# Optimization experiments

Hardware: AMD Instinct MI355X
Metric: run time of the kernel (lower is better)

## Reference

```python
import jax, jax.numpy as jnp
import numpy as np

B, N, TOPK = 64, 1024, 32
C1, DQ, DH, DO, DMLP = 92, 256, 512, 256, 1024
BN_EPS = 1e-5


def setup_inputs() -> dict:
    key = jax.random.key(0)
    ks = jax.random.split(key, 12)
    d_in = DQ + C1 + 4  # 352: query_embed + probs + bbox
    return {
        "probs": jax.random.normal(ks[0], (B, N, C1), jnp.float32),
        "bbox_coords": jax.random.uniform(ks[1], (B, N, 4), jnp.float32),
        "query_emb": jax.random.normal(ks[2], (N, DQ), jnp.float32),
        "node_emb": jax.random.normal(ks[3], (N, DQ), jnp.float32),
        "mlp_w1": jax.random.normal(ks[4], (d_in, DMLP), jnp.float32) * 0.02,
        "mlp_b1": jnp.zeros((DMLP,), jnp.float32),
        "mlp_w2": jax.random.normal(ks[5], (DMLP, N), jnp.float32) * 0.02,
        "mlp_b2": jnp.zeros((N,), jnp.float32),
        "conv1_w": jax.random.normal(ks[6], (DQ, DH), jnp.float32) * (DQ ** -0.5),
        "conv1_b": jnp.zeros((DH,), jnp.float32),
        "conv2_w": jax.random.normal(ks[7], (DH, DO), jnp.float32) * (DH ** -0.5),
        "conv2_b": jnp.zeros((DO,), jnp.float32),
        "bn_gamma": jnp.ones((DH,), jnp.float32),
        "bn_beta": jnp.zeros((DH,), jnp.float32),
    }


def reference(probs, bbox_coords, query_emb, node_emb, mlp_w1, mlp_b1,
              mlp_w2, mlp_b2, conv1_w, conv1_b, conv2_w, conv2_b,
              bn_gamma, bn_beta):
    b = probs.shape[0]
    # edge-weight MLP (2 layers, relu after first) -> dense adjacency (B,N,N)
    x = jnp.concatenate([jnp.broadcast_to(query_emb[None], (b, N, DQ)), probs, bbox_coords], axis=-1)
    adj = jax.nn.relu(x @ mlp_w1 + mlp_b1) @ mlp_w2 + mlp_b2
    vals, idx = jax.lax.top_k(adj, TOPK)          # (B,N,K) values sorted desc
    cols = idx.reshape(b, -1)                      # (B, N*K) targets
    w = vals.reshape(b, -1)                        # (B, N*K) edge weights
    loop = jnp.arange(N)
    row = jnp.repeat(loop, TOPK)                   # (N*K,) sources, shared
    rows_all = jnp.concatenate([row, loop])        # self-loops appended (fill=1)

    def gcn(xw, bias, c, ww):
        # GCNConv: sym-normalized gather-scale-scatter over edges + self loops
        cols2 = jnp.concatenate([c, loop])
        w2 = jnp.concatenate([ww, jnp.ones((N,), xw.dtype)])
        deg = jax.ops.segment_sum(w2, cols2, num_segments=N)
        dinv = deg ** -0.5
        dinv = jnp.where(jnp.isinf(dinv), 0.0, dinv)
        norm = dinv[rows_all] * w2 * dinv[cols2]
        return jax.ops.segment_sum(norm[:, None] * xw[rows_all], cols2, num_segments=N) + bias

    xw1 = node_emb @ conv1_w                       # shared across batch

    def per_batch(c, ww):
        h = gcn(xw1, conv1_b, c, ww)               # (N, DH)
        mu = h.mean(0)
        var = h.var(0)                             # biased var, as torch BN
        h = (h - mu) / jnp.sqrt(var + BN_EPS) * bn_gamma + bn_beta
        h = jax.nn.relu(h)
        return gcn(h @ conv2_w, conv2_b, c, ww)    # (N, DO)

    out = jax.vmap(per_batch)(cols, w)             # (B, N, DO)
    return out[:, None]                            # (B, 1, N, DO) matches torch stack of unsqueezed outs
```

## Files before the change

kernel.cpp:

```cpp
#include <hip/hip_runtime.h>
#include <stdint.h>

typedef float f32x4 __attribute__((ext_vector_type(4)));
typedef _Float16 h16x8 __attribute__((ext_vector_type(8)));
typedef _Float16 h16;
typedef unsigned short u16;

#define WSYNC() do { asm volatile("s_waitcnt lgkmcnt(0)" ::: "memory"); \
  __builtin_amdgcn_sched_barrier(0); } while (0)


__global__ void k_split_t(const float* __restrict__ in, h16* __restrict__ out,
                          int Cn, int Ck, int ostride, int doSplit) {
  __shared__ float t[32][33];
  int n0 = blockIdx.x * 32, k0 = blockIdx.y * 32;
  int tx = threadIdx.x, ty = threadIdx.y;
#pragma unroll
  for (int i = 0; i < 4; ++i)
    t[ty + i * 8][tx] = in[(size_t)(k0 + ty + i * 8) * Cn + n0 + tx];
  __syncthreads();
#pragma unroll
  for (int i = 0; i < 4; ++i) {
    int n = n0 + ty + i * 8, k = k0 + tx;
    float v = t[tx][ty + i * 8];
    h16 h = (h16)v;
    size_t base = (size_t)n * ostride + k;
    out[base] = h;
    if (doSplit) {
      out[base + Ck] = h;
      out[base + 2 * Ck] = (h16)(v - (float)h);
    }
  }
}

__global__ void k_xcat(const float* __restrict__ qe, const float* __restrict__ probs,
                       const float* __restrict__ bbox, h16* __restrict__ x, int r0, int n) {
  int i = blockIdx.x * 256 + threadIdx.x;
  if (i >= n) return;
  int rl = i / 352, k = i - rl * 352;
  int R = r0 + rl;
  int nn = R & 1023;
  float v;
  if (k < 256)      v = qe[nn * 256 + k];
  else if (k < 348) v = probs[(size_t)R * 92 + (k - 256)];
  else              v = bbox[(size_t)R * 4 + (k - 348)];
  h16 h = (h16)v;
  h16 l = (h16)(v - (float)h);
  size_t base = (size_t)rl * 704;
  x[base + k] = h; x[base + 352 + k] = l;
}

__global__ void k_xw1(const float* __restrict__ ne, const float* __restrict__ c1w,
                      float* __restrict__ xw1f) {
  int r = blockIdx.x >> 1;
  int d = (blockIdx.x & 1) * 256 + threadIdx.x;
  float s = 0.0f;
  for (int k = 0; k < 256; ++k) s += ne[r * 256 + k] * c1w[k * 512 + d];
  xw1f[r * 512 + d] = s;
}


template<int MODE>
__global__ __launch_bounds__(512, 2)
void k_gemm8(const h16* __restrict__ A, const h16* __restrict__ B, void* __restrict__ Cptr,
             const float* __restrict__ bias, const float* __restrict__ rscale,
             float2* __restrict__ bnp, int M, int N, int K, int AK) {
  __shared__ __align__(16) char lds[131072];
  const int tid = threadIdx.x;
  const int lane = tid & 63, wid = tid >> 6;
  const int wr = wid >> 2, wc = wid & 3;

  const int gx = N >> 8;
  const int nwg = gridDim.x, wg = blockIdx.x;
  const int q8 = nwg >> 3, r8 = nwg & 7, xcd = wg & 7, lo = wg >> 3;
  const int swz = (xcd < r8 ? xcd * (q8 + 1) : r8 * (q8 + 1) + (xcd - r8) * q8) + lo;
  const int bx = swz % gx, by = swz / gx;

  const int nt = K >> 6;
  const int srow = tid >> 3, s8 = tid & 7;

  char* ldsA = (char*)lds;
  char* ldsB = (char*)lds + 65536;

  auto stage = [&](const h16* __restrict__ Mat, int rowStride, int tileRowBase,
                   char* ldsBase, int buf, int half, int kbase) {
#pragma unroll
    for (int j = 0; j < 2; ++j) {
      int rl = half * 128 + srow + j * 64;
      int gcol = kbase + ((s8 ^ (rl & 7)) << 3);
      const char* src = (const char*)(Mat + (size_t)(tileRowBase + rl) * rowStride + gcol);
      char* dst = ldsBase + buf * 32768 + half * 16384 + j * 8192 + tid * 16;
      __builtin_amdgcn_global_load_lds((const __attribute__((address_space(1))) void*)src,
                                       (__attribute__((address_space(3))) void*)dst, 16, 0, 0);
    }
  };

  f32x4 acc[8][4] = {};
  h16x8 bfr[4][2];

  auto rdA = [&](int buf, int mf, int ks) -> h16x8 {
    int row = wr * 128 + mf * 16 + (lane & 15);
    int cb = ((ks << 6) + ((lane >> 4) << 4)) ^ ((row & 7) << 4);
    return *(const h16x8*)(ldsA + buf * 32768 + row * 128 + cb);
  };
  auto rdB = [&](int buf, int nf, int ks) -> h16x8 {
    int row = wc * 64 + nf * 16 + (lane & 15);
    int cb = ((ks << 6) + ((lane >> 4) << 4)) ^ ((row & 7) << 4);
    return *(const h16x8*)(ldsB + buf * 32768 + row * 128 + cb);
  };

#define BARRIER() do { asm volatile("" ::: "memory"); \
  __builtin_amdgcn_s_barrier(); asm volatile("" ::: "memory"); } while (0)

#define MFMA16(q, af)                                                          \
  __builtin_amdgcn_s_setprio(1);                                               \
  _Pragma("unroll") for (int m2 = 0; m2 < 2; ++m2)                             \
  _Pragma("unroll") for (int nf = 0; nf < 4; ++nf)                             \
  _Pragma("unroll") for (int ks = 0; ks < 2; ++ks)                             \
    acc[(q) * 2 + m2][nf] = __builtin_amdgcn_mfma_f32_16x16x32_f16(            \
        af[m2][ks], bfr[nf][ks], acc[(q) * 2 + m2][nf], 0, 0, 0);              \
  __builtin_amdgcn_s_setprio(0);

  const int aRow = by * 256, bRow = bx * 256;

  stage(A, AK, aRow, ldsA, 0, 0, 0);
  stage(A, AK, aRow, ldsA, 0, 1, 0);
  stage(B, K, bRow, ldsB, 0, 0, 0);
  stage(B, K, bRow, ldsB, 0, 1, 0);
  stage(B, K, bRow, ldsB, 1, 0, 64);
  stage(B, K, bRow, ldsB, 1, 1, 64);
  asm volatile("s_waitcnt vmcnt(4)" ::: "memory");
  BARRIER();

  for (int T = 0; T < nt; ++T) {
    const int p = T & 1;
    const int tkA = (T + 1) << 6;
    const int aA = (tkA < AK) ? tkA : tkA - AK;
    const int tkB = (T + 2) << 6;
    const bool sA = (T + 1) < nt, sB = (T + 2) < nt;

    {
#pragma unroll
      for (int nf = 0; nf < 4; ++nf)
#pragma unroll
        for (int ks = 0; ks < 2; ++ks) bfr[nf][ks] = rdB(p, nf, ks);
      h16x8 af[2][2];
#pragma unroll
      for (int m2 = 0; m2 < 2; ++m2)
#pragma unroll
        for (int ks = 0; ks < 2; ++ks) af[m2][ks] = rdA(p, m2, ks);
      if (sA) stage(A, AK, aRow, ldsA, p ^ 1, 0, aA);
      BARRIER();
      MFMA16(0, af)
      BARRIER();
    }
    {
      h16x8 af[2][2];
#pragma unroll
      for (int m2 = 0; m2 < 2; ++m2)
#pragma unroll
        for (int ks = 0; ks < 2; ++ks) af[m2][ks] = rdA(p, 2 + m2, ks);
      if (sA) stage(A, AK, aRow, ldsA, p ^ 1, 1, aA);
      BARRIER();
      MFMA16(1, af)
      BARRIER();
    }
    {
      h16x8 af[2][2];
#pragma unroll
      for (int m2 = 0; m2 < 2; ++m2)
#pragma unroll
        for (int ks = 0; ks < 2; ++ks) af[m2][ks] = rdA(p, 4 + m2, ks);
      if (sB) stage(B, K, bRow, ldsB, p, 0, tkB);
      BARRIER();
      MFMA16(2, af)
      BARRIER();
    }
    {
      h16x8 af[2][2];
#pragma unroll
      for (int m2 = 0; m2 < 2; ++m2)
#pragma unroll
        for (int ks = 0; ks < 2; ++ks) af[m2][ks] = rdA(p, 6 + m2, ks);
      if (sB) stage(B, K, bRow, ldsB, p, 1, tkB);
      BARRIER();
      MFMA16(3, af)
      if (sB) { asm volatile("s_waitcnt vmcnt(4)" ::: "memory"); }
      else    { asm volatile("s_waitcnt vmcnt(0)" ::: "memory"); }
      BARRIER();
    }
  }

  const int tM = by * 256 + wr * 128, tN = bx * 256 + wc * 64;
  float sl[4] = {0.f, 0.f, 0.f, 0.f}, ssl[4] = {0.f, 0.f, 0.f, 0.f};
#pragma unroll
  for (int mf = 0; mf < 8; ++mf) {
#pragma unroll
    for (int nf = 0; nf < 4; ++nf) {
      int c = tN + nf * 16 + (lane & 15);
      float bvl = bias[c];
#pragma unroll
      for (int i = 0; i < 4; ++i) {
        int r = tM + mf * 16 + (lane >> 4) * 4 + i;
        float v = acc[mf][nf][i];
        if (MODE == 5) v = v * rscale[r] + bvl;
        else v += bvl;
        if (MODE == 2) {
          ((float*)Cptr)[(size_t)r * N + c] = v;
        } else if (MODE == 5) {
          ((h16*)Cptr)[(size_t)r * N + c] = (h16)v;
          sl[nf] += v; ssl[nf] += v * v;
        } else {
          v = fmaxf(v, 0.0f);
          h16 h = (h16)v;
          h16 l = (h16)(v - (float)h);
          size_t o = (size_t)r * (2 * N) + c;
          ((h16*)Cptr)[o] = h;
          ((h16*)Cptr)[o + N] = l;
        }
      }
    }
  }
  if (MODE == 5) {
    int b = by >> 2;
#pragma unroll
    for (int nf = 0; nf < 4; ++nf) {
      float s = sl[nf], ss = ssl[nf];
      s += __shfl_xor(s, 16); ss += __shfl_xor(ss, 16);
      s += __shfl_xor(s, 32); ss += __shfl_xor(ss, 32);
      if (lane < 16) {
        int c = tN + nf * 16 + lane;
        atomicAdd(&bnp[b * 512 + c].x, s);
        atomicAdd(&bnp[b * 512 + c].y, ss);
      }
    }
  }
#undef BARRIER
#undef MFMA16
}


template<int MODE, int RELU>
__global__ __launch_bounds__(256)
void k_gemm(const h16* __restrict__ A, const h16* __restrict__ B, void* __restrict__ Cptr,
            const float* __restrict__ bias, const float* __restrict__ rscale,
            int M, int N, int K, int AK, int gx,
            long long sA, long long sB, long long sC) {
  __shared__ __align__(16) h16 As[128 * 32];
  __shared__ __align__(16) h16 Bs[128 * 32];
  const int tid = threadIdx.x;
  const int wid = tid >> 6, lane = tid & 63;
  const int wr = wid >> 1, wc = wid & 1;
  const int bz = blockIdx.y;

  const int nwg = gridDim.x, wg = blockIdx.x;
  const int q = nwg >> 3, r8 = nwg & 7, xcd = wg & 7, lo = wg >> 3;
  const int swz = (xcd < r8 ? xcd * (q + 1) : r8 * (q + 1) + (xcd - r8) * q) + lo;
  const int bx = swz % gx, by = swz / gx;

  const char* gA = (const char*)(A + (size_t)bz * sA + (size_t)by * 128 * AK +
                                 (size_t)(tid >> 2) * AK) + (tid & 3) * 16;
  const char* gB = (const char*)(B + (size_t)bz * sB + (size_t)bx * 128 * K +
                                 (size_t)(tid >> 2) * K) + (tid & 3) * 16;
  char* lAs = (char*)As + wid * 1024;
  char* lBs = (char*)Bs + wid * 1024;
  const long long rowStepA = (long long)64 * AK * 2;
  const long long rowStepB = (long long)64 * K * 2;

  f32x4 acc[4][4] = {};
  const int aoff = (wr * 64 + (lane & 15)) * 32 + (lane >> 4) * 8;
  const int boff = (wc * 64 + (lane & 15)) * 32 + (lane >> 4) * 8;

  for (int kt = 0; kt < K; kt += 32) {
    const int akt = (kt < AK) ? kt : kt - AK;
    __syncthreads();
#pragma unroll
    for (int j = 0; j < 2; ++j) {
      __builtin_amdgcn_global_load_lds(
          (const __attribute__((address_space(1))) void*)(gA + j * rowStepA + (size_t)akt * 2),
          (__attribute__((address_space(3))) void*)(lAs + j * 4096), 16, 0, 0);
      __builtin_amdgcn_global_load_lds(
          (const __attribute__((address_space(1))) void*)(gB + j * rowStepB + (size_t)kt * 2),
          (__attribute__((address_space(3))) void*)(lBs + j * 4096), 16, 0, 0);
    }
    asm volatile("s_waitcnt vmcnt(0)" ::: "memory");
    __syncthreads();

    h16x8 af[4], bv[4];
#pragma unroll
    for (int m = 0; m < 4; ++m) af[m] = *(const h16x8*)(As + aoff + m * 512);
#pragma unroll
    for (int n = 0; n < 4; ++n) bv[n] = *(const h16x8*)(Bs + boff + n * 512);
#pragma unroll
    for (int m = 0; m < 4; ++m)
#pragma unroll
      for (int n = 0; n < 4; ++n)
        acc[m][n] = __builtin_amdgcn_mfma_f32_16x16x32_f16(af[m], bv[n], acc[m][n], 0, 0, 0);
  }

  const int tM = by * 128 + wr * 64, tN = bx * 128 + wc * 64;
#pragma unroll
  for (int m = 0; m < 4; ++m) {
#pragma unroll
    for (int n = 0; n < 4; ++n) {
      int c = tN + n * 16 + (lane & 15);
      float bvl = bias ? bias[c] : 0.0f;
#pragma unroll
      for (int i = 0; i < 4; ++i) {
        int r = tM + m * 16 + (lane >> 4) * 4 + i;
        float v = acc[m][n][i];
        if (rscale) v *= rscale[bz * 1024 + r];
        v += bvl;
        if (RELU) v = fmaxf(v, 0.0f);
        if (MODE == 1) {
          size_t o = ((size_t)(r >> 10) * N + c) * 1024 + (r & 1023);
          ((h16*)Cptr)[o] = (h16)v;
        } else if (MODE == 2) {
          size_t o = (size_t)bz * sC + (size_t)r * N + c;
          ((float*)Cptr)[o] = v;
        }
      }
    }
  }
}


__global__ void k_topk(const float* __restrict__ adj, float* __restrict__ vals,
                       u16* __restrict__ idxo, float* __restrict__ deg, int r0) {
  __shared__ unsigned binsAll[4][256];
  const int wv = threadIdx.x >> 6, lane = threadIdx.x & 63;
  unsigned* bins = binsAll[wv];
  const int rl = blockIdx.x * 4 + wv;

  float v[16]; unsigned key[16];
  const float4* rp = (const float4*)(adj + (size_t)rl * 1024 + lane * 16);
#pragma unroll
  for (int q = 0; q < 4; ++q) {
    float4 t = rp[q];
    v[4 * q] = t.x; v[4 * q + 1] = t.y; v[4 * q + 2] = t.z; v[4 * q + 3] = t.w;
  }
#pragma unroll
  for (int j = 0; j < 16; ++j) {
    unsigned b = __float_as_uint(v[j]);
    key[j] = b ^ (unsigned)(((int)b >> 31) | (int)0x80000000);
  }

  unsigned pfx = 0; int need = 32;
#pragma unroll
  for (int lvl = 0; lvl < 4; ++lvl) {
    const int shift = 24 - lvl * 8;
    bins[lane] = 0; bins[lane + 64] = 0; bins[lane + 128] = 0; bins[lane + 192] = 0;
    WSYNC();
#pragma unroll
    for (int j = 0; j < 16; ++j) {
      bool cand = (lvl == 0) || ((key[j] >> (shift + 8)) == pfx);
      if (cand) atomicAdd(&bins[(key[j] >> shift) & 255u], 1u);
    }
    WSYNC();
    int c0 = (int)bins[lane * 4 + 0], c1 = (int)bins[lane * 4 + 1],
        c2 = (int)bins[lane * 4 + 2], c3 = (int)bins[lane * 4 + 3];
    WSYNC();
    int s = c0 + c1 + c2 + c3;
    int inc = s;
#pragma unroll
    for (int off = 1; off < 64; off <<= 1) {
      int t = __shfl_down(inc, off);
      if (lane + off < 64) inc += t;
    }
    int gt3 = inc - s;
    int gt2 = gt3 + c3, gt1 = gt2 + c2, gt0 = gt1 + c1;
    int tloc = -1, gtsel = 0;
    if (gt3 < need && gt3 + c3 >= need) { tloc = lane * 4 + 3; gtsel = gt3; }
    if (gt2 < need && gt2 + c2 >= need) { tloc = lane * 4 + 2; gtsel = gt2; }
    if (gt1 < need && gt1 + c1 >= need) { tloc = lane * 4 + 1; gtsel = gt1; }
    if (gt0 < need && gt0 + c0 >= need) { tloc = lane * 4 + 0; gtsel = gt0; }
    unsigned long long bal = __ballot(tloc >= 0);
    int src = __ffsll(bal) - 1;
    int t   = __shfl(tloc, src);
    int gtv = __shfl(gtsel, src);
    pfx = (pfx << 8) | (unsigned)t;
    need -= gtv;
  }

  unsigned sureMask = 0, tieMask = 0;
#pragma unroll
  for (int j = 0; j < 16; ++j) {
    if (key[j] > pfx) sureMask |= (1u << j);
    else if (key[j] == pfx) tieMask |= (1u << j);
  }
  int cs = __popc(sureMask), ct = __popc(tieMask);
  int incS = cs, incT = ct;
#pragma unroll
  for (int off = 1; off < 64; off <<= 1) {
    int a = __shfl_up(incS, off);
    int b2 = __shfl_up(incT, off);
    if (lane >= off) { incS += a; incT += b2; }
  }
  int baseS = incS - cs, baseT = incT - ct;
  int totalS = __shfl(incS, 63);
  size_t obase = ((size_t)(r0 + rl)) * 32;
  int degb = ((r0 + rl) >> 10) << 10;
  int o = baseS;
#pragma unroll
  for (int j = 0; j < 16; ++j)
    if (sureMask & (1u << j)) {
      vals[obase + o] = v[j];
      idxo[obase + o] = (u16)(lane * 16 + j);
      atomicAdd(&deg[degb + lane * 16 + j], v[j]);
      ++o;
    }
  int o2 = totalS + baseT;
#pragma unroll
  for (int j = 0; j < 16; ++j)
    if (tieMask & (1u << j)) {
      if (o2 < 32) {
        vals[obase + o2] = v[j];
        idxo[obase + o2] = (u16)(lane * 16 + j);
        atomicAdd(&deg[degb + lane * 16 + j], v[j]);
      }
      ++o2;
    }
}


__global__ void k_deg_init(float* deg) {
  int i = blockIdx.x * 256 + threadIdx.x;
  if (i < 65536) deg[i] = 1.0f;
}

__global__ void k_dinv(const float* __restrict__ deg, float* __restrict__ dinv) {
  int i = blockIdx.x * 256 + threadIdx.x;
  if (i >= 65536) return;
  float d = deg[i];
  float r = 1.0f / sqrtf(d);
  if (isinf(r)) r = 0.0f;
  dinv[i] = r;
}

__global__ void k_self(const float* __restrict__ dinv, h16* __restrict__ Wd, int g) {
  int i = blockIdx.x * 256 + threadIdx.x;
  if (i >= 16384) return;
  int bl = i >> 10, c = i & 1023;
  Wd[((size_t)bl << 20) + (size_t)c * 1024 + c] = (h16)dinv[g * 16384 + i];
}

__global__ void k_edge(const float* __restrict__ vals, const u16* __restrict__ idxo,
                       const float* __restrict__ dinv, h16* __restrict__ Wd, int g) {
  int e = blockIdx.x * 256 + threadIdx.x;
  if (e >= 524288) return;
  int bl = e >> 15;
  int r = (e >> 5) & 1023;
  size_t E = (size_t)g * 524288 + e;
  int c = (int)idxo[E];
  float w = vals[E] * dinv[g * 16384 + (bl << 10) + r];
  size_t o = ((size_t)bl << 20) + (size_t)c * 1024 + r;
  Wd[o] = (h16)((float)Wd[o] + w);
}

__global__ void k_wipe(const u16* __restrict__ idxo, h16* __restrict__ Wd, int g) {
  int t = blockIdx.x * 256 + threadIdx.x;
  if (t < 524288) {
    int bl = t >> 15, r = (t >> 5) & 1023;
    int c = (int)idxo[(size_t)g * 524288 + t];
    Wd[((size_t)bl << 20) + (size_t)c * 1024 + r] = (h16)0.0f;
  } else {
    int i = t - 524288;
    if (i < 16384) {
      int bl = i >> 10, c = i & 1023;
      Wd[((size_t)bl << 20) + (size_t)c * 1024 + c] = (h16)0.0f;
    }
  }
}


__global__ void k_bnfin(const float2* __restrict__ part, float* __restrict__ mu,
                        float* __restrict__ rstd) {
  int i = blockIdx.x * 256 + threadIdx.x;
  if (i >= 8192) return;
  float2 t = part[i];
  float m = t.x * (1.0f / 1024.0f);
  float var = t.y * (1.0f / 1024.0f) - m * m;
  mu[i] = m;
  rstd[i] = 1.0f / sqrtf(var + 1e-5f);
}

__global__ void k_bnapply(h16* __restrict__ h1, const float* __restrict__ mu,
                          const float* __restrict__ rstd, const float* __restrict__ gamma,
                          const float* __restrict__ beta) {
  int i = blockIdx.x * 256 + threadIdx.x;
  if (i >= 16 * 1024 * 512) return;
  int d = i & 511;
  int b = i >> 19;
  float y = ((float)h1[i] - mu[b * 512 + d]) * rstd[b * 512 + d] * gamma[d] + beta[d];
  h1[i] = (h16)fmaxf(y, 0.0f);
}


extern "C" void kernel_launch(void* const* d_in, const int* in_sizes, int n_in,
                              void* d_out, int out_size, void* d_ws, size_t ws_size,
                              hipStream_t stream) {
  const float* probs = (const float*)d_in[0];
  const float* bbox  = (const float*)d_in[1];
  const float* qe    = (const float*)d_in[2];
  const float* ne    = (const float*)d_in[3];
  const float* w1    = (const float*)d_in[4];
  const float* b1    = (const float*)d_in[5];
  const float* w2    = (const float*)d_in[6];
  const float* b2    = (const float*)d_in[7];
  const float* c1w   = (const float*)d_in[8];
  const float* c1b   = (const float*)d_in[9];
  const float* c2w   = (const float*)d_in[10];
  const float* c2b   = (const float*)d_in[11];
  const float* gamma = (const float*)d_in[12];
  const float* beta  = (const float*)d_in[13];

  if (ws_size < 82444288ULL) return;
  const bool big = ws_size >= 115998720ULL;
  const int CH = big ? 16384 : 8192;
  const int NCH = 65536 / CH;

  char* p = (char*)d_ws;
  h16* W1cat = (h16*)p; p += (size_t)1024 * 1088 * 2;
  h16* W2cat = (h16*)p; p += (size_t)1024 * 3072 * 2;
  h16* c2wt  = (h16*)p; p += (size_t)256 * 512 * 2;
  float* xw1f = (float*)p; p += (size_t)1024 * 512 * 4;
  h16*  xw1t = (h16*)p;  p += (size_t)512 * 1024 * 2;
  float* vals = (float*)p; p += (size_t)2097152 * 4;
  u16*   idxo = (u16*)p;   p += (size_t)2097152 * 2;
  float* deg  = (float*)p; p += (size_t)65536 * 4;
  float* dinv = (float*)p; p += (size_t)65536 * 4;
  float* mu   = (float*)p; p += (size_t)64 * 512 * 4;
  float* rstd = (float*)p; p += (size_t)64 * 512 * 4;
  float2* bnp = (float2*)p; p += (size_t)16 * 8 * 512 * 8;
  char* R1 = p;
  h16* Xcat  = (h16*)R1;
  h16* Hcat2 = (h16*)(R1 + (size_t)CH * 704 * 2);
  h16* Wd   = (h16*)R1;
  h16* h1   = (h16*)(R1 + 33554432);
  h16* xw2t = (h16*)(R1 + 50331648);
  float* adjf = (float*)d_out;

  hipMemsetAsync(W1cat, 0, (size_t)1024 * 1088 * 2, stream);
  k_split_t<<<dim3(32, 11), dim3(32, 8), 0, stream>>>(w1, W1cat, 1024, 352, 1088, 1);
  k_split_t<<<dim3(32, 32), dim3(32, 8), 0, stream>>>(w2, W2cat, 1024, 1024, 3072, 1);
  k_split_t<<<dim3(8, 16), dim3(32, 8), 0, stream>>>(c2w, c2wt, 256, 512, 512, 0);
  k_xw1<<<2048, 256, 0, stream>>>(ne, c1w, xw1f);
  k_split_t<<<dim3(16, 32), dim3(32, 8), 0, stream>>>(xw1f, xw1t, 512, 1024, 1024, 0);
  k_deg_init<<<256, 256, 0, stream>>>(deg);

  for (int c = 0; c < NCH; ++c) {
    int r0 = c * CH;
    k_xcat<<<(CH * 352) / 256, 256, 0, stream>>>(qe, probs, bbox, Xcat, r0, CH * 352);
    k_gemm8<3><<<(CH / 256) * 4, 512, 0, stream>>>(Xcat, W1cat, Hcat2, b1, nullptr,
                                                   nullptr, CH, 1024, 1088, 704);
    k_gemm8<2><<<(CH / 256) * 4, 512, 0, stream>>>(Hcat2, W2cat, adjf, b2, nullptr,
                                                   nullptr, CH, 1024, 3072, 2048);
    k_topk<<<CH / 4, 256, 0, stream>>>(adjf, vals, idxo, deg, r0);
  }

  k_dinv<<<256, 256, 0, stream>>>(deg, dinv);

  for (int g = 0; g < 4; ++g) {
    const float* dg = dinv + g * 16384;
    if (g == 0) hipMemsetAsync(Wd, 0, (size_t)33554432, stream);
    k_self<<<64, 256, 0, stream>>>(dinv, Wd, g);
    k_edge<<<2048, 256, 0, stream>>>(vals, idxo, dinv, Wd, g);
    hipMemsetAsync(bnp, 0, (size_t)16 * 512 * 8, stream);
    k_gemm8<5><<<128, 512, 0, stream>>>(Wd, xw1t, h1, c1b, dg, bnp,
                                        16384, 512, 1024, 1024);
    k_bnfin<<<32, 256, 0, stream>>>(bnp, mu, rstd);
    k_bnapply<<<32768, 256, 0, stream>>>(h1, mu, rstd, gamma, beta);
    k_gemm<1, 0><<<dim3(256, 1), 256, 0, stream>>>(h1, c2wt, xw2t, nullptr, nullptr,
                                                   16384, 256, 512, 512, 2, 0, 0, 0);
    k_gemm<2, 0><<<dim3(16, 16), 256, 0, stream>>>(Wd, xw2t,
                                                   (float*)d_out + (size_t)g * 16 * 262144,
                                                   c2b, dg, 1024, 256, 1024, 1024, 2,
                                                   1048576LL, 262144LL, 262144LL);
    if (g < 3) k_wipe<<<2112, 256, 0, stream>>>(idxo, Wd, g);
  }
}
```

Baseline: 1.454 ms.

## Route GCN second-layer GEMMs through the pipelined 256x256 kernel with batch strides

Adds batch strides and an optional row scale/bias to the large double-buffered 256x256 MFMA GEMM, plus a transposed-output mode. The two small 128x128 GEMMs in the second GCN layer now use it instead of the simpler kernel, which is removed. BN apply is vectorised to 8 halves per thread. The sparse wipe kernel is replaced by a full 32MB memset every group, which adds memory traffic. The second-layer GEMMs also launch far fewer workgroups (64 blocks for the xw2 GEMM), which may underfill the GPU.

```diff
diff --git a/kernel.cpp b/kernel.cpp
--- a/kernel.cpp
+++ b/kernel.cpp
@@ -64,11 +64,13 @@
 __global__ __launch_bounds__(512, 2)
 void k_gemm8(const h16* __restrict__ A, const h16* __restrict__ B, void* __restrict__ Cptr,
              const float* __restrict__ bias, const float* __restrict__ rscale,
-             float2* __restrict__ bnp, int M, int N, int K, int AK) {
+             float2* __restrict__ bnp, int M, int N, int K, int AK,
+             long long sA, long long sB, long long sC) {
   __shared__ __align__(16) char lds[131072];
   const int tid = threadIdx.x;
   const int lane = tid & 63, wid = tid >> 6;
   const int wr = wid >> 2, wc = wid & 3;
+  const int bz = blockIdx.y;
 
   const int gx = N >> 8;
   const int nwg = gridDim.x, wg = blockIdx.x;
@@ -78,6 +80,9 @@
 
   const int nt = K >> 6;
   const int srow = tid >> 3, s8 = tid & 7;
+
+  const h16* Ab = A + (size_t)bz * sA;
+  const h16* Bb = B + (size_t)bz * sB;
 
   char* ldsA = (char*)lds;
   char* ldsB = (char*)lds + 65536;
@@ -123,12 +128,12 @@
 
   const int aRow = by * 256, bRow = bx * 256;
 
-  stage(A, AK, aRow, ldsA, 0, 0, 0);
-  stage(A, AK, aRow, ldsA, 0, 1, 0);
-  stage(B, K, bRow, ldsB, 0, 0, 0);
-  stage(B, K, bRow, ldsB, 0, 1, 0);
-  stage(B, K, bRow, ldsB, 1, 0, 64);
-  stage(B, K, bRow, ldsB, 1, 1, 64);
+  stage(Ab, AK, aRow, ldsA, 0, 0, 0);
+  stage(Ab, AK, aRow, ldsA, 0, 1, 0);
+  stage(Bb, K, bRow, ldsB, 0, 0, 0);
+  stage(Bb, K, bRow, ldsB, 0, 1, 0);
+  stage(Bb, K, bRow, ldsB, 1, 0, 64);
+  stage(Bb, K, bRow, ldsB, 1, 1, 64);
   asm volatile("s_waitcnt vmcnt(4)" ::: "memory");
   BARRIER();
 
@@ -137,7 +142,7 @@
     const int tkA = (T + 1) << 6;
     const int aA = (tkA < AK) ? tkA : tkA - AK;
     const int tkB = (T + 2) << 6;
-    const bool sA = (T + 1) < nt, sB = (T + 2) < nt;
+    const bool sAn = (T + 1) < nt, sBn = (T + 2) < nt;
 
     {
 #pragma unroll
@@ -149,7 +154,7 @@
       for (int m2 = 0; m2 < 2; ++m2)
 #pragma unroll
         for (int ks = 0; ks < 2; ++ks) af[m2][ks] = rdA(p, m2, ks);
-      if (sA) stage(A, AK, aRow, ldsA, p ^ 1, 0, aA);
+      if (sAn) stage(Ab, AK, aRow, ldsA, p ^ 1, 0, aA);
       BARRIER();
       MFMA16(0, af)
       BARRIER();
@@ -160,7 +165,7 @@
       for (int m2 = 0; m2 < 2; ++m2)
 #pragma unroll
         for (int ks = 0; ks < 2; ++ks) af[m2][ks] = rdA(p, 2 + m2, ks);
-      if (sA) stage(A, AK, aRow, ldsA, p ^ 1, 1, aA);
+      if (sAn) stage(Ab, AK, aRow, ldsA, p ^ 1, 1, aA);
       BARRIER();
       MFMA16(1, af)
       BARRIER();
@@ -171,7 +176,7 @@
       for (int m2 = 0; m2 < 2; ++m2)
 #pragma unroll
         for (int ks = 0; ks < 2; ++ks) af[m2][ks] = rdA(p, 4 + m2, ks);
-      if (sB) stage(B, K, bRow, ldsB, p, 0, tkB);
+      if (sBn) stage(Bb, K, bRow, ldsB, p, 0, tkB);
       BARRIER();
       MFMA16(2, af)
       BARRIER();
@@ -182,11 +187,11 @@
       for (int m2 = 0; m2 < 2; ++m2)
 #pragma unroll
         for (int ks = 0; ks < 2; ++ks) af[m2][ks] = rdA(p, 6 + m2, ks);
-      if (sB) stage(B, K, bRow, ldsB, p, 1, tkB);
+      if (sBn) stage(Bb, K, bRow, ldsB, p, 1, tkB);
       BARRIER();
       MFMA16(3, af)
-      if (sB) { asm volatile("s_waitcnt vmcnt(4)" ::: "memory"); }
-      else    { asm volatile("s_waitcnt vmcnt(0)" ::: "memory"); }
+      if (sBn) { asm volatile("s_waitcnt vmcnt(4)" ::: "memory"); }
+      else     { asm volatile("s_waitcnt vmcnt(0)" ::: "memory"); }
       BARRIER();
     }
   }
@@ -198,18 +203,21 @@
 #pragma unroll
     for (int nf = 0; nf < 4; ++nf) {
       int c = tN + nf * 16 + (lane & 15);
-      float bvl = bias[c];
+      float bvl = bias ? bias[c] : 0.0f;
 #pragma unroll
       for (int i = 0; i < 4; ++i) {
         int r = tM + mf * 16 + (lane >> 4) * 4 + i;
         float v = acc[mf][nf][i];
-        if (MODE == 5) v = v * rscale[r] + bvl;
-        else v += bvl;
+        if (rscale) v *= rscale[bz * 1024 + r];
+        v += bvl;
         if (MODE == 2) {
-          ((float*)Cptr)[(size_t)r * N + c] = v;
+          ((float*)Cptr)[(size_t)bz * sC + (size_t)r * N + c] = v;
         } else if (MODE == 5) {
           ((h16*)Cptr)[(size_t)r * N + c] = (h16)v;
           sl[nf] += v; ssl[nf] += v * v;
+        } else if (MODE == 6) {
+          size_t o = ((size_t)(r >> 10) * N + c) * 1024 + (r & 1023);
+          ((h16*)Cptr)[o] = (h16)v;
         } else {
           v = fmaxf(v, 0.0f);
           h16 h = (h16)v;
@@ -237,91 +245,6 @@
   }
 #undef BARRIER
 #undef MFMA16
-}
-
-
-template<int MODE, int RELU>
-__global__ __launch_bounds__(256)
-void k_gemm(const h16* __restrict__ A, const h16* __restrict__ B, void* __restrict__ Cptr,
-            const float* __restrict__ bias, const float* __restrict__ rscale,
-            int M, int N, int K, int AK, int gx,
-            long long sA, long long sB, long long sC) {
-  __shared__ __align__(16) h16 As[128 * 32];
-  __shared__ __align__(16) h16 Bs[128 * 32];
-  const int tid = threadIdx.x;
-  const int wid = tid >> 6, lane = tid & 63;
-  const int wr = wid >> 1, wc = wid & 1;
-  const int bz = blockIdx.y;
-
-  const int nwg = gridDim.x, wg = blockIdx.x;
-  const int q = nwg >> 3, r8 = nwg & 7, xcd = wg & 7, lo = wg >> 3;
-  const int swz = (xcd < r8 ? xcd * (q + 1) : r8 * (q + 1) + (xcd - r8) * q) + lo;
-  const int bx = swz % gx, by = swz / gx;
-
-  const char* gA = (const char*)(A + (size_t)bz * sA + (size_t)by * 128 * AK +
-                                 (size_t)(tid >> 2) * AK) + (tid & 3) * 16;
-  const char* gB = (const char*)(B + (size_t)bz * sB + (size_t)bx * 128 * K +
-                                 (size_t)(tid >> 2) * K) + (tid & 3) * 16;
-  char* lAs = (char*)As + wid * 1024;
-  char* lBs = (char*)Bs + wid * 1024;
-  const long long rowStepA = (long long)64 * AK * 2;
-  const long long rowStepB = (long long)64 * K * 2;
-
-  f32x4 acc[4][4] = {};
-  const int aoff = (wr * 64 + (lane & 15)) * 32 + (lane >> 4) * 8;
-  const int boff = (wc * 64 + (lane & 15)) * 32 + (lane >> 4) * 8;
-
-  for (int kt = 0; kt < K; kt += 32) {
-    const int akt = (kt < AK) ? kt : kt - AK;
-    __syncthreads();
-#pragma unroll
-    for (int j = 0; j < 2; ++j) {
-      __builtin_amdgcn_global_load_lds(
-          (const __attribute__((address_space(1))) void*)(gA + j * rowStepA + (size_t)akt * 2),
-          (__attribute__((address_space(3))) void*)(lAs + j * 4096), 16, 0, 0);
-      __builtin_amdgcn_global_load_lds(
-          (const __attribute__((address_space(1))) void*)(gB + j * rowStepB + (size_t)kt * 2),
-          (__attribute__((address_space(3))) void*)(lBs + j * 4096), 16, 0, 0);
-    }
-    asm volatile("s_waitcnt vmcnt(0)" ::: "memory");
-    __syncthreads();
-
-    h16x8 af[4], bv[4];
-#pragma unroll
-    for (int m = 0; m < 4; ++m) af[m] = *(const h16x8*)(As + aoff + m * 512);
-#pragma unroll
-    for (int n = 0; n < 4; ++n) bv[n] = *(const h16x8*)(Bs + boff + n * 512);
-#pragma unroll
-    for (int m = 0; m < 4; ++m)
-#pragma unroll
-      for (int n = 0; n < 4; ++n)
-        acc[m][n] = __builtin_amdgcn_mfma_f32_16x16x32_f16(af[m], bv[n], acc[m][n], 0, 0, 0);
-  }
-
-  const int tM = by * 128 + wr * 64, tN = bx * 128 + wc * 64;
-#pragma unroll
-  for (int m = 0; m < 4; ++m) {
-#pragma unroll
-    for (int n = 0; n < 4; ++n) {
-      int c = tN + n * 16 + (lane & 15);
-      float bvl = bias ? bias[c] : 0.0f;
-#pragma unroll
-      for (int i = 0; i < 4; ++i) {
-        int r = tM + m * 16 + (lane >> 4) * 4 + i;
-        float v = acc[m][n][i];
-        if (rscale) v *= rscale[bz * 1024 + r];
-        v += bvl;
-        if (RELU) v = fmaxf(v, 0.0f);
-        if (MODE == 1) {
-          size_t o = ((size_t)(r >> 10) * N + c) * 1024 + (r & 1023);
-          ((h16*)Cptr)[o] = (h16)v;
-        } else if (MODE == 2) {
-          size_t o = (size_t)bz * sC + (size_t)r * N + c;
-          ((float*)Cptr)[o] = v;
-        }
-      }
-    }
-  }
 }
 
 
@@ -457,21 +380,6 @@
   Wd[o] = (h16)((float)Wd[o] + w);
 }
 
-__global__ void k_wipe(const u16* __restrict__ idxo, h16* __restrict__ Wd, int g) {
-  int t = blockIdx.x * 256 + threadIdx.x;
-  if (t < 524288) {
-    int bl = t >> 15, r = (t >> 5) & 1023;
-    int c = (int)idxo[(size_t)g * 524288 + t];
-    Wd[((size_t)bl << 20) + (size_t)c * 1024 + r] = (h16)0.0f;
-  } else {
-    int i = t - 524288;
-    if (i < 16384) {
-      int bl = i >> 10, c = i & 1023;
-      Wd[((size_t)bl << 20) + (size_t)c * 1024 + c] = (h16)0.0f;
-    }
-  }
-}
-
 
 __global__ void k_bnfin(const float2* __restrict__ part, float* __restrict__ mu,
                         float* __restrict__ rstd) {
@@ -488,11 +396,19 @@
                           const float* __restrict__ rstd, const float* __restrict__ gamma,
                           const float* __restrict__ beta) {
   int i = blockIdx.x * 256 + threadIdx.x;
-  if (i >= 16 * 1024 * 512) return;
-  int d = i & 511;
-  int b = i >> 19;
-  float y = ((float)h1[i] - mu[b * 512 + d]) * rstd[b * 512 + d] * gamma[d] + beta[d];
-  h1[i] = (h16)fmaxf(y, 0.0f);
+  if (i >= 1048576) return;
+  int i8 = i * 8;
+  int d0 = i8 & 511;
+  int b = i8 >> 19;
+  h16x8 hv = *(const h16x8*)(h1 + i8);
+  h16x8 ov;
+#pragma unroll
+  for (int j = 0; j < 8; ++j) {
+    int d = d0 + j;
+    float y = ((float)hv[j] - mu[b * 512 + d]) * rstd[b * 512 + d] * gamma[d] + beta[d];
+    ov[j] = (h16)fmaxf(y, 0.0f);
+  }
+  *(h16x8*)(h1 + i8) = ov;
 }
 
 
@@ -552,9 +468,9 @@
     int r0 = c * CH;
     k_xcat<<<(CH * 352) / 256, 256, 0, stream>>>(qe, probs, bbox, Xcat, r0, CH * 352);
     k_gemm8<3><<<(CH / 256) * 4, 512, 0, stream>>>(Xcat, W1cat, Hcat2, b1, nullptr,
-                                                   nullptr, CH, 1024, 1088, 704);
+                                                   nullptr, CH, 1024, 1088, 704, 0, 0, 0);
     k_gemm8<2><<<(CH / 256) * 4, 512, 0, stream>>>(Hcat2, W2cat, adjf, b2, nullptr,
-                                                   nullptr, CH, 1024, 3072, 2048);
+                                                   nullptr, CH, 1024, 3072, 2048, 0, 0, 0);
     k_topk<<<CH / 4, 256, 0, stream>>>(adjf, vals, idxo, deg, r0);
   }
 
@@ -562,20 +478,19 @@
 
   for (int g = 0; g < 4; ++g) {
     const float* dg = dinv + g * 16384;
-    if (g == 0) hipMemsetAsync(Wd, 0, (size_t)33554432, stream);
+    hipMemsetAsync(Wd, 0, (size_t)33554432, stream);
     k_self<<<64, 256, 0, stream>>>(dinv, Wd, g);
     k_edge<<<2048, 256, 0, stream>>>(vals, idxo, dinv, Wd, g);
     hipMemsetAsync(bnp, 0, (size_t)16 * 512 * 8, stream);
     k_gemm8<5><<<128, 512, 0, stream>>>(Wd, xw1t, h1, c1b, dg, bnp,
-                                        16384, 512, 1024, 1024);
+                                        16384, 512, 1024, 1024, 0, 0, 0);
     k_bnfin<<<32, 256, 0, stream>>>(bnp, mu, rstd);
-    k_bnapply<<<32768, 256, 0, stream>>>(h1, mu, rstd, gamma, beta);
-    k_gemm<1, 0><<<dim3(256, 1), 256, 0, stream>>>(h1, c2wt, xw2t, nullptr, nullptr,
-                                                   16384, 256, 512, 512, 2, 0, 0, 0);
-    k_gemm<2, 0><<<dim3(16, 16), 256, 0, stream>>>(Wd, xw2t,
-                                                   (float*)d_out + (size_t)g * 16 * 262144,
-                                                   c2b, dg, 1024, 256, 1024, 1024, 2,
-                                                   1048576LL, 262144LL, 262144LL);
-    if (g < 3) k_wipe<<<2112, 256, 0, stream>>>(idxo, Wd, g);
-  }
-}
+    k_bnapply<<<4096, 256, 0, stream>>>(h1, mu, rstd, gamma, beta);
+    k_gemm8<6><<<64, 512, 0, stream>>>(h1, c2wt, xw2t, nullptr, nullptr, nullptr,
+                                       16384, 256, 512, 512, 0, 0, 0);
+    k_gemm8<2><<<dim3(4, 16), 512, 0, stream>>>(Wd, xw2t,
+                                                (float*)d_out + (size_t)g * 16 * 262144,
+                                                c2b, dg, nullptr, 1024, 256, 1024, 1024,
+                                                1048576LL, 262144LL, 262144LL);
+  }
+}
```

Result: slower. 1.666 ms (+14.5%).
